# Performance work log

Measured on AMD Instinct MI355X. Metric: run time of the kernel, lower is better.

Reference implementation:

```python
import jax, jax.numpy as jnp
import numpy as np

D, B, N = 8, 16, 2048  # delays, batch, neurons


def setup_inputs() -> dict:
    key = jax.random.key(0)
    ks = jax.random.split(key, 7)
    return {
        "W": jax.random.normal(ks[0], (N, N), dtype=jnp.float32),
        "Wlong": jax.random.normal(ks[1], (B, N, N), dtype=jnp.float32),
        "Wshort": jax.random.normal(ks[2], (D, B, N), dtype=jnp.float32),
        "Xd": jax.random.uniform(ks[3], (D, B, N), dtype=jnp.float32),
        "delaymap": jax.random.uniform(ks[4], (D, N, N), dtype=jnp.float32),
        "STDP_frac": jax.random.uniform(ks[5], (N, N), dtype=jnp.float32),
        "signs_pre": jax.random.normal(ks[6], (N,), dtype=jnp.float32),
    }


def reference(W, Wlong, Wshort, Xd, delaymap, STDP_frac, signs_pre):
    # align_signs: per-pre-neuron sign, zeroed where W <= 0  -> (e, o)
    signs = jnp.where(W > 0, jnp.sign(signs_pre)[:, None], jnp.zeros((), W.dtype))
    # STDP blend: W_eff[b,e,o] = signs * (W*(1-frac) + Wlong*frac)
    Weff = signs[None] * (W[None] * (1.0 - STDP_frac)[None] + Wlong * STDP_frac[None])
    # STP modulation: Wshort + 1  -> (d, b, e)
    Ws = Wshort + 1.0
    # fused 4-operand delay contraction -> synaptic current (b, o)
    I = jnp.einsum('beo,dbe,deo,dbe->bo', Weff, Xd, delaymap, Ws)
    return I
```

## Files before the change

### kernel.cpp

```cpp
#include <hip/hip_runtime.h>

#define Nn 2048
#define Bb 16
#define Dd 8
#define BN (Bb * Nn)
#define NN ((size_t)Nn * Nn)
#define EC 4
#define ECH (Nn / EC)

#define XW_BYTES   ((size_t)Nn * Bb * Dd * 4)
#define PART_BYTES ((size_t)ECH * BN * 4)
#define RCG 8

typedef float v4f __attribute__((ext_vector_type(4)));

__global__ void prep_kernel(const float* __restrict__ Xd,
                            const float* __restrict__ Wshort,
                            float* __restrict__ xw,
                            float* __restrict__ out) {
    int t = blockIdx.x * blockDim.x + threadIdx.x;
    if (t >= BN) return;
    out[t] = 0.0f;
    int b = t >> 11;
    int e = t & (Nn - 1);
    float v[Dd];
#pragma unroll
    for (int d = 0; d < Dd; ++d) {
        int idx = d * BN + b * Nn + e;
        v[d] = Xd[idx] * (Wshort[idx] + 1.0f);
    }
    v4f* dst = (v4f*)(xw + (size_t)e * (Bb * Dd) + b * Dd);
    dst[0] = (v4f){v[0], v[1], v[2], v[3]};
    dst[1] = (v4f){v[4], v[5], v[6], v[7]};
}

template <bool USE_PART>
__global__ __launch_bounds__(256) void main_kernel(
        const float* __restrict__ W,
        const float* __restrict__ Wlong,
        const float* __restrict__ delaymap,
        const float* __restrict__ frac,
        const float* __restrict__ signs_pre,
        const float* __restrict__ xw,
        float* __restrict__ partial,
        float* __restrict__ out) {
    const int o = (blockIdx.x * 256 + threadIdx.x) * 4;
    const int chunk = blockIdx.y;
    const int e0 = chunk * EC;

    v4f acc[Bb];
#pragma unroll
    for (int b = 0; b < Bb; ++b) acc[b] = (v4f)0.0f;

#pragma unroll
    for (int ei = 0; ei < EC; ++ei) {
        const int e = e0 + ei;
        const float sp = signs_pre[e];
        const float sgn = (sp > 0.0f) ? 1.0f : ((sp < 0.0f) ? -1.0f : 0.0f);

        const size_t eo = (size_t)e * Nn + o;
        const v4f w  = *(const v4f*)(W + eo);
        const v4f fr = *(const v4f*)(frac + eo);

        v4f dm[Dd];
#pragma unroll
        for (int d = 0; d < Dd; ++d)
            dm[d] = *(const v4f*)(delaymap + (size_t)d * NN + eo);

        v4f sg, base;
#pragma unroll
        for (int c = 0; c < 4; ++c) {
            sg[c]   = (w[c] > 0.0f) ? sgn : 0.0f;
            base[c] = w[c] * (1.0f - fr[c]);
        }

        const float* xwe = xw + (size_t)e * (Bb * Dd);

#pragma unroll
        for (int b = 0; b < Bb; ++b) {
            const v4f wl = *(const v4f*)(Wlong + (size_t)b * NN + eo);
            v4f inner = (v4f)0.0f;
#pragma unroll
            for (int d = 0; d < Dd; ++d)
                inner += dm[d] * xwe[b * Dd + d];
            const v4f weff = sg * (base + wl * fr);
            acc[b] += weff * inner;
        }
    }

    if (USE_PART) {
        float* pbase = partial + (size_t)chunk * BN + o;
#pragma unroll
        for (int b = 0; b < Bb; ++b)
            *(v4f*)(pbase + b * Nn) = acc[b];
    } else {
#pragma unroll
        for (int b = 0; b < Bb; ++b) {
            float* op = out + b * Nn + o;
            atomicAdd(op + 0, acc[b][0]);
            atomicAdd(op + 1, acc[b][1]);
            atomicAdd(op + 2, acc[b][2]);
            atomicAdd(op + 3, acc[b][3]);
        }
    }
}

__global__ __launch_bounds__(256) void reduce_kernel(
        const float* __restrict__ partial, float* __restrict__ out) {
    const int t = blockIdx.x * 256 + threadIdx.x;
    const int cg = blockIdx.y;
    const int c0 = cg * (ECH / RCG);
    float s0 = 0.f, s1 = 0.f, s2 = 0.f, s3 = 0.f;
#pragma unroll 4
    for (int c = c0; c < c0 + (ECH / RCG); c += 4) {
        s0 += partial[(size_t)(c + 0) * BN + t];
        s1 += partial[(size_t)(c + 1) * BN + t];
        s2 += partial[(size_t)(c + 2) * BN + t];
        s3 += partial[(size_t)(c + 3) * BN + t];
    }
    atomicAdd(out + t, (s0 + s1) + (s2 + s3));
}

extern "C" void kernel_launch(void* const* d_in, const int* in_sizes, int n_in,
                              void* d_out, int out_size, void* d_ws, size_t ws_size,
                              hipStream_t stream) {
    const float* W         = (const float*)d_in[0];
    const float* Wlong     = (const float*)d_in[1];
    const float* Wshort    = (const float*)d_in[2];
    const float* Xd        = (const float*)d_in[3];
    const float* delaymap  = (const float*)d_in[4];
    const float* frac      = (const float*)d_in[5];
    const float* signs_pre = (const float*)d_in[6];
    float* out = (float*)d_out;
    float* xw  = (float*)d_ws;
    float* partial = (float*)((char*)d_ws + XW_BYTES);

    prep_kernel<<<BN / 256, 256, 0, stream>>>(Xd, Wshort, xw, out);

    dim3 grid(Nn / (256 * 4), ECH);
    if (ws_size >= XW_BYTES + PART_BYTES) {
        main_kernel<true><<<grid, 256, 0, stream>>>(W, Wlong, delaymap, frac,
                                                    signs_pre, xw, partial, out);
        dim3 rgrid(BN / 256, RCG);
        reduce_kernel<<<rgrid, 256, 0, stream>>>(partial, out);
    } else {
        main_kernel<false><<<grid, 256, 0, stream>>>(W, Wlong, delaymap, frac,
                                                     signs_pre, xw, partial, out);
    }
}
```

Measured before the change: 503.5 us.

## Stage per-chunk xw in shared memory, double e-chunk size, batch Wlong loads

Each block now handles 8 presynaptic neurons instead of 4, which halves the number of partial sums written and later reduced. The block's slice of the xw table is staged in LDS once per block rather than read from global memory per thread. The e-loop is no longer unrolled, the batch loop issues four Wlong loads at a time, and the launch bounds request two blocks per SM. The risks are lower unrolling and extra register pressure from the grouped loads, which could reduce memory-level parallelism.

```diff
diff --git a/kernel.cpp b/kernel.cpp
--- a/kernel.cpp
+++ b/kernel.cpp
@@ -5,7 +5,7 @@
 #define Dd 8
 #define BN (Bb * Nn)
 #define NN ((size_t)Nn * Nn)
-#define EC 4
+#define EC 8
 #define ECH (Nn / EC)
 
 #define XW_BYTES   ((size_t)Nn * Bb * Dd * 4)
@@ -35,7 +35,7 @@
 }
 
 template <bool USE_PART>
-__global__ __launch_bounds__(256) void main_kernel(
+__global__ __launch_bounds__(256, 2) void main_kernel(
         const float* __restrict__ W,
         const float* __restrict__ Wlong,
         const float* __restrict__ delaymap,
@@ -48,24 +48,31 @@
     const int chunk = blockIdx.y;
     const int e0 = chunk * EC;
 
+    __shared__ float sxw[EC * Bb * Dd];
+    {
+        const v4f* src = (const v4f*)(xw + (size_t)e0 * (Bb * Dd));
+        ((v4f*)sxw)[threadIdx.x] = src[threadIdx.x];
+    }
+    __syncthreads();
+
     v4f acc[Bb];
 #pragma unroll
     for (int b = 0; b < Bb; ++b) acc[b] = (v4f)0.0f;
 
-#pragma unroll
+#pragma unroll 1
     for (int ei = 0; ei < EC; ++ei) {
         const int e = e0 + ei;
-        const float sp = signs_pre[e];
-        const float sgn = (sp > 0.0f) ? 1.0f : ((sp < 0.0f) ? -1.0f : 0.0f);
+        const size_t eo = (size_t)e * Nn + o;
 
-        const size_t eo = (size_t)e * Nn + o;
         const v4f w  = *(const v4f*)(W + eo);
         const v4f fr = *(const v4f*)(frac + eo);
-
         v4f dm[Dd];
 #pragma unroll
         for (int d = 0; d < Dd; ++d)
             dm[d] = *(const v4f*)(delaymap + (size_t)d * NN + eo);
+
+        const float sp = signs_pre[e];
+        const float sgn = (sp > 0.0f) ? 1.0f : ((sp < 0.0f) ? -1.0f : 0.0f);
 
         v4f sg, base;
 #pragma unroll
@@ -74,17 +81,30 @@
             base[c] = w[c] * (1.0f - fr[c]);
         }
 
-        const float* xwe = xw + (size_t)e * (Bb * Dd);
+        const float* xwe = sxw + ei * (Bb * Dd);
 
 #pragma unroll
-        for (int b = 0; b < Bb; ++b) {
-            const v4f wl = *(const v4f*)(Wlong + (size_t)b * NN + eo);
-            v4f inner = (v4f)0.0f;
+        for (int bg = 0; bg < Bb; bg += 4) {
+            const v4f wl0 = *(const v4f*)(Wlong + (size_t)(bg + 0) * NN + eo);
+            const v4f wl1 = *(const v4f*)(Wlong + (size_t)(bg + 1) * NN + eo);
+            const v4f wl2 = *(const v4f*)(Wlong + (size_t)(bg + 2) * NN + eo);
+            const v4f wl3 = *(const v4f*)(Wlong + (size_t)(bg + 3) * NN + eo);
+
+            v4f in0 = dm[0] * xwe[(bg + 0) * Dd + 0];
+            v4f in1 = dm[0] * xwe[(bg + 1) * Dd + 0];
+            v4f in2 = dm[0] * xwe[(bg + 2) * Dd + 0];
+            v4f in3 = dm[0] * xwe[(bg + 3) * Dd + 0];
 #pragma unroll
-            for (int d = 0; d < Dd; ++d)
-                inner += dm[d] * xwe[b * Dd + d];
-            const v4f weff = sg * (base + wl * fr);
-            acc[b] += weff * inner;
+            for (int d = 1; d < Dd; ++d) {
+                in0 += dm[d] * xwe[(bg + 0) * Dd + d];
+                in1 += dm[d] * xwe[(bg + 1) * Dd + d];
+                in2 += dm[d] * xwe[(bg + 2) * Dd + d];
+                in3 += dm[d] * xwe[(bg + 3) * Dd + d];
+            }
+            acc[bg + 0] += sg * (base + wl0 * fr) * in0;
+            acc[bg + 1] += sg * (base + wl1 * fr) * in1;
+            acc[bg + 2] += sg * (base + wl2 * fr) * in2;
+            acc[bg + 3] += sg * (base + wl3 * fr) * in3;
         }
     }
 
```

Result: faster. 480.1 us (-4.7%).

## Double-buffer per-row loads, stage xw in LDS, and double the e-chunk

Applied to the files above, without the earlier changes.

Each block now handles eight pre-neuron rows instead of four, which halves the partial buffer written and re-read by the reduction. The block's xw slice is staged in shared memory, and the W, frac and delaymap loads for the next row are software-prefetched while the current row is computed. The inner loop is no longer unrolled and a min-waves hint is added to launch_bounds. The prefetch buffers and the sixteen-entry Wlong register array raise register pressure, which may cap occupancy or cause spills.

```diff
diff --git a/kernel.cpp b/kernel.cpp
--- a/kernel.cpp
+++ b/kernel.cpp
@@ -5,7 +5,7 @@
 #define Dd 8
 #define BN (Bb * Nn)
 #define NN ((size_t)Nn * Nn)
-#define EC 4
+#define EC 8
 #define ECH (Nn / EC)
 
 #define XW_BYTES   ((size_t)Nn * Bb * Dd * 4)
@@ -35,7 +35,7 @@
 }
 
 template <bool USE_PART>
-__global__ __launch_bounds__(256) void main_kernel(
+__global__ __launch_bounds__(256, 2) void main_kernel(
         const float* __restrict__ W,
         const float* __restrict__ Wlong,
         const float* __restrict__ delaymap,
@@ -48,24 +48,47 @@
     const int chunk = blockIdx.y;
     const int e0 = chunk * EC;
 
+    __shared__ float sxw[EC * Bb * Dd];
+    {
+        const v4f* src = (const v4f*)(xw + (size_t)e0 * (Bb * Dd));
+        ((v4f*)sxw)[threadIdx.x] = src[threadIdx.x];
+    }
+    __syncthreads();
+
     v4f acc[Bb];
 #pragma unroll
     for (int b = 0; b < Bb; ++b) acc[b] = (v4f)0.0f;
 
-#pragma unroll
-    for (int ei = 0; ei < EC; ++ei) {
-        const int e = e0 + ei;
-        const float sp = signs_pre[e];
-        const float sgn = (sp > 0.0f) ? 1.0f : ((sp < 0.0f) ? -1.0f : 0.0f);
-
-        const size_t eo = (size_t)e * Nn + o;
-        const v4f w  = *(const v4f*)(W + eo);
-        const v4f fr = *(const v4f*)(frac + eo);
-
-        v4f dm[Dd];
+    v4f w, fr, dm[Dd];
+    {
+        const size_t eo = (size_t)e0 * Nn + o;
+        w  = *(const v4f*)(W + eo);
+        fr = *(const v4f*)(frac + eo);
 #pragma unroll
         for (int d = 0; d < Dd; ++d)
             dm[d] = *(const v4f*)(delaymap + (size_t)d * NN + eo);
+    }
+
+#pragma unroll 1
+    for (int ei = 0; ei < EC; ++ei) {
+        const int e = e0 + ei;
+        const size_t eo = (size_t)e * Nn + o;
+
+        v4f wl[Bb];
+#pragma unroll
+        for (int b = 0; b < Bb; ++b)
+            wl[b] = *(const v4f*)(Wlong + (size_t)b * NN + eo);
+
+        const size_t eon = eo + ((ei < EC - 1) ? (size_t)Nn : 0);
+        v4f wn  = *(const v4f*)(W + eon);
+        v4f frn = *(const v4f*)(frac + eon);
+        v4f dmn[Dd];
+#pragma unroll
+        for (int d = 0; d < Dd; ++d)
+            dmn[d] = *(const v4f*)(delaymap + (size_t)d * NN + eon);
+
+        const float sp = signs_pre[e];
+        const float sgn = (sp > 0.0f) ? 1.0f : ((sp < 0.0f) ? -1.0f : 0.0f);
 
         v4f sg, base;
 #pragma unroll
@@ -74,18 +97,21 @@
             base[c] = w[c] * (1.0f - fr[c]);
         }
 
-        const float* xwe = xw + (size_t)e * (Bb * Dd);
+        const float* xwe = sxw + ei * (Bb * Dd);
 
 #pragma unroll
         for (int b = 0; b < Bb; ++b) {
-            const v4f wl = *(const v4f*)(Wlong + (size_t)b * NN + eo);
-            v4f inner = (v4f)0.0f;
+            v4f inner = dm[0] * xwe[b * Dd + 0];
 #pragma unroll
-            for (int d = 0; d < Dd; ++d)
+            for (int d = 1; d < Dd; ++d)
                 inner += dm[d] * xwe[b * Dd + d];
-            const v4f weff = sg * (base + wl * fr);
-            acc[b] += weff * inner;
+            acc[b] += sg * (base + wl[b] * fr) * inner;
         }
+
+        w = wn;
+        fr = frn;
+#pragma unroll
+        for (int d = 0; d < Dd; ++d) dm[d] = dmn[d];
     }
 
     if (USE_PART) {
```

Result: faster. 483.4 us (-4.0%).

## Split batch across blocks, stage xw in LDS, double e-chunk size

Applied to the files above, without the earlier changes.

Each block now handles half the batch (8 of 16) for a block of output columns, with the grid's x dimension doubled to cover both halves, and the e-chunk grows from 4 to 8 rows. The xw coefficients for the chunk are staged once in shared memory instead of being read from global memory per element. The e loop is no longer unrolled, and launch bounds request 3 blocks per SM, to cut register pressure and raise occupancy. As a trade-off, W, frac and delaymap are now loaded twice, once per batch half, and the reduce kernel's chunk count per group changes with the new EC.

```diff
diff --git a/kernel.cpp b/kernel.cpp
--- a/kernel.cpp
+++ b/kernel.cpp
@@ -3,9 +3,10 @@
 #define Nn 2048
 #define Bb 16
 #define Dd 8
+#define BH 8
 #define BN (Bb * Nn)
 #define NN ((size_t)Nn * Nn)
-#define EC 4
+#define EC 8
 #define ECH (Nn / EC)
 
 #define XW_BYTES   ((size_t)Nn * Bb * Dd * 4)
@@ -13,6 +14,7 @@
 #define RCG 8
 
 typedef float v4f __attribute__((ext_vector_type(4)));
+typedef float v2f __attribute__((ext_vector_type(2)));
 
 __global__ void prep_kernel(const float* __restrict__ Xd,
                             const float* __restrict__ Wshort,
@@ -35,7 +37,7 @@
 }
 
 template <bool USE_PART>
-__global__ __launch_bounds__(256) void main_kernel(
+__global__ __launch_bounds__(256, 3) void main_kernel(
         const float* __restrict__ W,
         const float* __restrict__ Wlong,
         const float* __restrict__ delaymap,
@@ -44,28 +46,46 @@
         const float* __restrict__ xw,
         float* __restrict__ partial,
         float* __restrict__ out) {
-    const int o = (blockIdx.x * 256 + threadIdx.x) * 4;
+    const int bh = blockIdx.x & 1;
+    const int ob = blockIdx.x >> 1;
+    const int o = (ob * 256 + threadIdx.x) * 4;
     const int chunk = blockIdx.y;
     const int e0 = chunk * EC;
+    const int b0 = bh * BH;
 
-    v4f acc[Bb];
+    __shared__ float sxw[EC * BH * Dd];
+    {
+        const int e_local = threadIdx.x >> 5;
+        const int lane32  = threadIdx.x & 31;
+        const v2f* src = (const v2f*)(xw + (size_t)(e0 + e_local) * (Bb * Dd)
+                                      + b0 * Dd);
+        ((v2f*)sxw)[threadIdx.x] = src[lane32];
+    }
+    __syncthreads();
+
+    v4f acc[BH];
 #pragma unroll
-    for (int b = 0; b < Bb; ++b) acc[b] = (v4f)0.0f;
+    for (int b = 0; b < BH; ++b) acc[b] = (v4f)0.0f;
 
-#pragma unroll
+#pragma unroll 1
     for (int ei = 0; ei < EC; ++ei) {
         const int e = e0 + ei;
-        const float sp = signs_pre[e];
-        const float sgn = (sp > 0.0f) ? 1.0f : ((sp < 0.0f) ? -1.0f : 0.0f);
+        const size_t eo = (size_t)e * Nn + o;
 
-        const size_t eo = (size_t)e * Nn + o;
         const v4f w  = *(const v4f*)(W + eo);
         const v4f fr = *(const v4f*)(frac + eo);
-
         v4f dm[Dd];
 #pragma unroll
         for (int d = 0; d < Dd; ++d)
             dm[d] = *(const v4f*)(delaymap + (size_t)d * NN + eo);
+
+        v4f wl[BH];
+#pragma unroll
+        for (int b = 0; b < BH; ++b)
+            wl[b] = *(const v4f*)(Wlong + (size_t)(b0 + b) * NN + eo);
+
+        const float sp = signs_pre[e];
+        const float sgn = (sp > 0.0f) ? 1.0f : ((sp < 0.0f) ? -1.0f : 0.0f);
 
         v4f sg, base;
 #pragma unroll
@@ -74,29 +94,27 @@
             base[c] = w[c] * (1.0f - fr[c]);
         }
 
-        const float* xwe = xw + (size_t)e * (Bb * Dd);
+        const float* xwe = sxw + ei * (BH * Dd);
 
 #pragma unroll
-        for (int b = 0; b < Bb; ++b) {
-            const v4f wl = *(const v4f*)(Wlong + (size_t)b * NN + eo);
-            v4f inner = (v4f)0.0f;
+        for (int b = 0; b < BH; ++b) {
+            v4f inner = dm[0] * xwe[b * Dd + 0];
 #pragma unroll
-            for (int d = 0; d < Dd; ++d)
+            for (int d = 1; d < Dd; ++d)
                 inner += dm[d] * xwe[b * Dd + d];
-            const v4f weff = sg * (base + wl * fr);
-            acc[b] += weff * inner;
+            acc[b] += sg * (base + wl[b] * fr) * inner;
         }
     }
 
     if (USE_PART) {
-        float* pbase = partial + (size_t)chunk * BN + o;
+        float* pbase = partial + (size_t)chunk * BN + (size_t)b0 * Nn + o;
 #pragma unroll
-        for (int b = 0; b < Bb; ++b)
+        for (int b = 0; b < BH; ++b)
             *(v4f*)(pbase + b * Nn) = acc[b];
     } else {
 #pragma unroll
-        for (int b = 0; b < Bb; ++b) {
-            float* op = out + b * Nn + o;
+        for (int b = 0; b < BH; ++b) {
+            float* op = out + (b0 + b) * Nn + o;
             atomicAdd(op + 0, acc[b][0]);
             atomicAdd(op + 1, acc[b][1]);
             atomicAdd(op + 2, acc[b][2]);
@@ -137,7 +155,7 @@
 
     prep_kernel<<<BN / 256, 256, 0, stream>>>(Xd, Wshort, xw, out);
 
-    dim3 grid(Nn / (256 * 4), ECH);
+    dim3 grid(4, ECH);
     if (ws_size >= XW_BYTES + PART_BYTES) {
         main_kernel<true><<<grid, 256, 0, stream>>>(W, Wlong, delaymap, frac,
                                                     signs_pre, xw, partial, out);
```

Measured after the change: 489.5 us. 1.03x faster.
